# Kernel tuning notes

Hardware: AMD Instinct MI355X
Metric: run time of the kernel (lower is better)

Reference implementation:

```python
import jax, jax.numpy as jnp
import numpy as np

N, M = 50000, 12
ORIG, NBR_F, AF = 92, 41, 64
B, NA = 500, 100
NCONV = 3
BN_EPS = 1e-5


def _batchnorm(x, g, b):
    # training-mode batchnorm over axis 0 (biased variance, like torch)
    mu = jnp.mean(x, axis=0)
    var = jnp.mean((x - mu) ** 2, axis=0)
    return (x - mu) * jax.lax.rsqrt(var + BN_EPS) * g + b


def _conv_layer(atom, nbr_fea, nbr_idx, W, bW, g1, b1, g2, b2):
    n, m = nbr_idx.shape
    atom_nbr = atom[nbr_idx]                                   # [N,M,AF] gather
    center = jnp.broadcast_to(atom[:, None, :], (n, m, AF))
    total = jnp.concatenate([center, atom_nbr, nbr_fea], axis=2)  # [N,M,2AF+NBR_F]
    gated = jnp.einsum('nmf,of->nmo', total, W) + bW              # [N,M,2AF]
    gated = _batchnorm(gated.reshape(-1, 2 * AF), g1, b1).reshape(n, m, 2 * AF)
    filt, core = gated[..., :AF], gated[..., AF:]
    summed = jnp.sum(jax.nn.sigmoid(filt) * jax.nn.softplus(core), axis=1)  # [N,AF]
    summed = _batchnorm(summed, g2, b2)
    return jax.nn.softplus(atom + summed)


def setup_inputs() -> dict:
    key = jax.random.key(0)
    ks = jax.random.split(key, 12)
    inp = {
        'atom_fea': jax.random.normal(ks[0], (N, ORIG), jnp.float32),
        'nbr_fea': jax.random.normal(ks[1], (N, M, NBR_F), jnp.float32),
        'nbr_fea_idx': jax.random.randint(ks[2], (N, M), 0, N, jnp.int32),
        'crystal_atom_idx': jnp.arange(B * NA, dtype=jnp.int32).reshape(B, NA),
        'mask': jnp.ones((ORIG,), jnp.float32),
        'emb_W': jax.random.normal(ks[3], (AF, ORIG), jnp.float32) * 0.05,
        'conv_W': jax.random.normal(ks[4], (NCONV, 2 * AF, 2 * AF + NBR_F), jnp.float32) * 0.05,
        'conv_b': jnp.zeros((NCONV, 2 * AF), jnp.float32),
        'bn1_g': jnp.ones((NCONV, 2 * AF), jnp.float32),
        'bn1_b': jnp.zeros((NCONV, 2 * AF), jnp.float32),
        'bn2_g': jnp.ones((NCONV, AF), jnp.float32),
        'bn2_b': jnp.zeros((NCONV, AF), jnp.float32),
        'fc1_W': jax.random.normal(ks[5], (AF, AF), jnp.float32) * 0.05,
        'fc1_b': jnp.zeros((AF,), jnp.float32),
        'fc2_W': jax.random.normal(ks[6], (AF, AF), jnp.float32) * 0.05,
        'fc2_b': jnp.zeros((AF,), jnp.float32),
        'out_W': jax.random.normal(ks[7], (1, AF), jnp.float32) * 0.05,
        'out_b': jnp.zeros((1,), jnp.float32),
    }
    return inp


def reference(atom_fea, nbr_fea, nbr_fea_idx, crystal_atom_idx, mask, emb_W,
              conv_W, conv_b, bn1_g, bn1_b, bn2_g, bn2_b,
              fc1_W, fc1_b, fc2_W, fc2_b, out_W, out_b):
    x = atom_fea * mask                      # learned input mask
    atom_mask_feature = x
    h = x @ emb_W.T                          # embedding, no bias -> [N,AF]
    for i in range(NCONV):
        h = _conv_layer(h, nbr_fea, nbr_fea_idx, conv_W[i], conv_b[i],
                        bn1_g[i], bn1_b[i], bn2_g[i], bn2_b[i])
    g = h[crystal_atom_idx]                  # [B,NA,AF]
    norm = jnp.sqrt(jnp.sum(g * g, axis=-1, keepdims=True))
    g = g / jnp.maximum(norm, 1e-12)         # F.normalize p=2
    pooled = jnp.mean(g, axis=1)             # [B,AF]
    z = jax.nn.softplus(pooled @ fc1_W.T + fc1_b)
    z = jax.nn.softplus(z @ fc2_W.T + fc2_b)
    props = z @ out_W.T + out_b              # [B,1]
    return props, atom_mask_feature
```

## Files before the change

kernel.cpp:

```cpp
#include <hip/hip_runtime.h>
#include <hip/hip_bf16.h>
#include <stdint.h>

#define NN      50000
#define MMN     12
#define NMROWS  600000
#define ORIGF   92
#define NBRF    41
#define AFD     64
#define GCH     128
#define KTOT    169
#define BBC     500
#define NAA     100
#define BN_EPS  1e-5f
#define GROWS   96

typedef unsigned short u16;
typedef __attribute__((ext_vector_type(8))) short bf16x8;
typedef __attribute__((ext_vector_type(4))) float f32x4;

__device__ __forceinline__ float b2f(u16 u) {
    union { uint32_t i; float f; } v; v.i = ((uint32_t)u) << 16; return v.f;
}
__device__ __forceinline__ float hi2f(uint32_t p) {
    union { uint32_t i; float f; } v; v.i = p & 0xffff0000u; return v.f;
}
__device__ __forceinline__ u16 f2b(float f) {
    __hip_bfloat16 h = __float2bfloat16(f);
    return *(u16*)&h;
}
__device__ __forceinline__ float sp_f(float x) {
    return fmaxf(x, 0.f) + __logf(1.f + __expf(-fabsf(x)));
}
__device__ __forceinline__ float sigm_f(float x) {
    return __builtin_amdgcn_rcpf(1.f + __expf(-x));
}

__global__ void k_mask(const float* __restrict__ atom, const float* __restrict__ mask,
                       float* __restrict__ dout) {
    int i = blockIdx.x * blockDim.x + threadIdx.x;
    int stride = gridDim.x * blockDim.x;
    for (; i < NN * ORIGF; i += stride) {
        int k = i % ORIGF;
        dout[BBC + i] = atom[i] * mask[k];
    }
}

__global__ __launch_bounds__(256, 2) void k_emb(const float* __restrict__ atom,
                                                const float* __restrict__ mask,
                                                const float* __restrict__ embW,
                                                u16* __restrict__ h) {
    __shared__ float xs[4 * 96];
    int lane = threadIdx.x & 63;
    int w = threadIdx.x >> 6;
    float wr[ORIGF];
#pragma unroll
    for (int k = 0; k < ORIGF; ++k) wr[k] = embW[lane * ORIGF + k];
    float m1 = mask[lane];
    float m2 = (lane < ORIGF - 64) ? mask[64 + lane] : 0.f;
    for (int base = blockIdx.x * 4; base < NN; base += gridDim.x * 4) {
        int n = base + w;
        xs[w * 96 + lane] = atom[(size_t)n * ORIGF + lane] * m1;
        if (lane < ORIGF - 64)
            xs[w * 96 + 64 + lane] = atom[(size_t)n * ORIGF + 64 + lane] * m2;
        __syncthreads();
        float acc = 0.f;
#pragma unroll
        for (int k4 = 0; k4 < ORIGF / 4; ++k4) {
            float4 f = *(const float4*)&xs[w * 96 + 4 * k4];
            acc += f.x * wr[4*k4] + f.y * wr[4*k4+1] + f.z * wr[4*k4+2] + f.w * wr[4*k4+3];
        }
        h[(size_t)n * AFD + lane] = f2b(acc);
        __syncthreads();
    }
}

__global__ __launch_bounds__(256, 2) void k_cn(const u16* __restrict__ h,
                                               const float* __restrict__ convW,
                                               uint32_t* __restrict__ C32) {
    __shared__ float xs[2 * AFD];
    int lane = threadIdx.x & 63;
    int w = threadIdx.x >> 6;
    int half = w & 1;
    int sub = w >> 1;
    int koff = half * AFD;
    float wa[AFD], wb[AFD];
#pragma unroll
    for (int k = 0; k < AFD; ++k) {
        wa[k] = convW[lane * KTOT + koff + k];
        wb[k] = convW[(lane + 64) * KTOT + koff + k];
    }
    for (int base = blockIdx.x * 2; base < NN; base += gridDim.x * 2) {
        int n = base + sub;
        if (half == 0) xs[sub * AFD + lane] = b2f(h[(size_t)n * AFD + lane]);
        __syncthreads();
        float aa = 0.f, ab = 0.f;
#pragma unroll
        for (int k4 = 0; k4 < AFD / 4; ++k4) {
            float4 f = *(const float4*)&xs[sub * AFD + 4 * k4];
            aa += f.x * wa[4*k4] + f.y * wa[4*k4+1] + f.z * wa[4*k4+2] + f.w * wa[4*k4+3];
            ab += f.x * wb[4*k4] + f.y * wb[4*k4+1] + f.z * wb[4*k4+2] + f.w * wb[4*k4+3];
        }
        C32[(size_t)n * 128 + half * 64 + lane] = (uint32_t)f2b(aa) | ((uint32_t)f2b(ab) << 16);
        __syncthreads();
    }
}

__device__ __forceinline__ void stage_nbrf(const float* nbrf, int r0, float* fs) {
    const float4* src = (const float4*)(nbrf + (size_t)r0 * NBRF);
    for (int t = threadIdx.x; t < (GROWS * NBRF) / 4; t += 256) {
        float4 f = src[t];
        float vals[4] = {f.x, f.y, f.z, f.w};
#pragma unroll
        for (int j = 0; j < 4; ++j) {
            int e = t * 4 + j;
            int row = e / NBRF;
            int k = e - row * NBRF;
            fs[row * 44 + k] = vals[j];
        }
    }
}

template<bool STORE>
__global__ __launch_bounds__(256, 4) void k_gs3(
    const uint32_t* __restrict__ C32, const float* __restrict__ nbrf,
    const int* __restrict__ nbridx, const float* __restrict__ convW,
    const float* __restrict__ convb, float* __restrict__ stats,
    uint32_t* __restrict__ gated32)
{
    __shared__ __align__(16) u16 As[GROWS * 72];
    __shared__ __align__(16) u16 Ws[GCH * 72];
    __shared__ int nidx[GROWS];
    const int tid = threadIdx.x;
    const int lane = tid & 63;
    const int w = tid >> 6;
    const int lr = lane & 15;
    const int lg = lane >> 4;
    const int r0 = blockIdx.x * GROWS;
    const int nbase = blockIdx.x * (GROWS / MMN);

    const float* src = nbrf + (size_t)r0 * NBRF;
    for (int e = tid; e < GROWS * NBRF; e += 256) {
        int row = e / NBRF, k = e - row * NBRF;
        As[row * 72 + k] = f2b(src[e]);
    }
    for (int e = tid; e < GROWS * 23; e += 256) {
        int row = e / 23, k = 41 + (e - row * 23);
        As[row * 72 + k] = (k == 41) ? (u16)0x3F80 : (u16)0;
    }
    for (int e = tid; e < GCH * NBRF; e += 256) {
        int ch = e / NBRF, k = e - ch * NBRF;
        Ws[ch * 72 + k] = f2b(convW[ch * KTOT + 128 + k]);
    }
    for (int e = tid; e < GCH * 23; e += 256) {
        int ch = e / 23, k = 41 + (e - ch * 23);
        Ws[ch * 72 + k] = (k == 41) ? f2b(convb[ch]) : (u16)0;
    }
    if (tid < GROWS) nidx[tid] = nbridx[r0 + tid];
    __syncthreads();

    const u16* wlo = &Ws[(w * 16 + lr) * 72 + 8 * lg];
    const u16* whi = &Ws[(64 + w * 16 + lr) * 72 + 8 * lg];
    bf16x8 bl0 = *(const bf16x8*)(wlo);
    bf16x8 bl1 = *(const bf16x8*)(wlo + 32);
    bf16x8 bh0 = *(const bf16x8*)(whi);
    bf16x8 bh1 = *(const bf16x8*)(whi + 32);

    f32x4 acc[6][2];
    const f32x4 z = {0.f, 0.f, 0.f, 0.f};
#pragma unroll
    for (int mt = 0; mt < 6; ++mt) {
        const u16* ap = &As[(mt * 16 + lr) * 72 + 8 * lg];
        bf16x8 a0 = *(const bf16x8*)(ap);
        bf16x8 a1 = *(const bf16x8*)(ap + 32);
        acc[mt][0] = __builtin_amdgcn_mfma_f32_16x16x32_bf16(a1, bl1,
                     __builtin_amdgcn_mfma_f32_16x16x32_bf16(a0, bl0, z, 0, 0, 0), 0, 0, 0);
        acc[mt][1] = __builtin_amdgcn_mfma_f32_16x16x32_bf16(a1, bh1,
                     __builtin_amdgcn_mfma_f32_16x16x32_bf16(a0, bh0, z, 0, 0, 0), 0, 0, 0);
    }

    const int word = w * 16 + lr;
    float slo = 0.f, qlo = 0.f, shi = 0.f, qhi = 0.f;
#pragma unroll
    for (int mt = 0; mt < 6; ++mt) {
        uint32_t p1[4], p2[4];
#pragma unroll
        for (int rg = 0; rg < 4; ++rg) {
            int row = mt * 16 + 4 * lg + rg;
            int n = nbase + row / MMN;
            int j = nidx[row];
            p1[rg] = C32[(size_t)n * 128 + word];
            p2[rg] = C32[(size_t)j * 128 + 64 + word];
        }
#pragma unroll
        for (int rg = 0; rg < 4; ++rg) {
            float glo = acc[mt][0][rg] + b2f((u16)p1[rg]) + b2f((u16)p2[rg]);
            float ghi = acc[mt][1][rg] + hi2f(p1[rg]) + hi2f(p2[rg]);
            if (STORE) {
                int row = mt * 16 + 4 * lg + rg;
                gated32[(size_t)(r0 + row) * 64 + word] =
                    (uint32_t)f2b(glo) | ((uint32_t)f2b(ghi) << 16);
            }
            slo += glo; qlo = fmaf(glo, glo, qlo);
            shi += ghi; qhi = fmaf(ghi, ghi, qhi);
        }
    }
    slo += __shfl_xor(slo, 16, 64); slo += __shfl_xor(slo, 32, 64);
    qlo += __shfl_xor(qlo, 16, 64); qlo += __shfl_xor(qlo, 32, 64);
    shi += __shfl_xor(shi, 16, 64); shi += __shfl_xor(shi, 32, 64);
    qhi += __shfl_xor(qhi, 16, 64); qhi += __shfl_xor(qhi, 32, 64);
    if (lane < 16) {
        atomicAdd(&stats[word], slo);
        atomicAdd(&stats[128 + word], qlo);
        atomicAdd(&stats[64 + word], shi);
        atomicAdd(&stats[128 + 64 + word], qhi);
    }
}

__global__ void k_fin(float* __restrict__ stats, const float* __restrict__ gg,
                      const float* __restrict__ bb, int nch, float invcnt,
                      int sumoff, int sqoff, int scoff, int shoff) {
    int c = threadIdx.x;
    if (c < nch) {
        float mean = stats[sumoff + c] * invcnt;
        float var  = fmaxf(stats[sqoff + c] * invcnt - mean * mean, 0.f);
        float sc   = gg[c] * rsqrtf(var + BN_EPS);
        stats[scoff + c] = sc;
        stats[shoff + c] = bb[c] - mean * sc;
    }
}

__global__ __launch_bounds__(256) void k_acts(
    const uint32_t* __restrict__ gated32, float* __restrict__ stats,
    u16* __restrict__ summed)
{
    __shared__ float red[4][64][2];
    int lane = threadIdx.x & 63;
    int w = threadIdx.x >> 6;
    float sa = stats[384 + lane],      ba = stats[512 + lane];
    float sb = stats[384 + 64 + lane], bb = stats[512 + 64 + lane];
    int wave = blockIdx.x * 4 + w, nw = gridDim.x * 4;
    float s2 = 0.f, q2 = 0.f;
    for (int n = wave; n < NN; n += nw) {
        const uint32_t* gr = gated32 + (size_t)n * MMN * 64;
        float s = 0.f;
#pragma unroll
        for (int m = 0; m < MMN; ++m) {
            uint32_t p = gr[m * 64 + lane];
            float f1 = b2f((u16)p) * sa + ba;
            float cc = hi2f(p) * sb + bb;
            s += sigm_f(f1) * sp_f(cc);
        }
        summed[(size_t)n * AFD + lane] = f2b(s);
        s2 += s; q2 += s * s;
    }
    red[w][lane][0] = s2; red[w][lane][1] = q2;
    __syncthreads();
    if (threadIdx.x < 64) {
        int c = threadIdx.x;
        float a = 0, b = 0;
#pragma unroll
        for (int ww = 0; ww < 4; ++ww) { a += red[ww][c][0]; b += red[ww][c][1]; }
        atomicAdd(&stats[256 + c], a);
        atomicAdd(&stats[320 + c], b);
    }
}

__device__ __forceinline__ void edge_dot(const float* fr, const float* wfa,
                                         const float* wfb, float& aa, float& ab) {
#pragma unroll
    for (int k4 = 0; k4 < 10; ++k4) {
        float4 f = *(const float4*)&fr[4 * k4];
        aa += f.x * wfa[4*k4] + f.y * wfa[4*k4+1] + f.z * wfa[4*k4+2] + f.w * wfa[4*k4+3];
        ab += f.x * wfb[4*k4] + f.y * wfb[4*k4+1] + f.z * wfb[4*k4+2] + f.w * wfb[4*k4+3];
    }
    aa += fr[40] * wfa[40];
    ab += fr[40] * wfb[40];
}

__global__ __launch_bounds__(256) void k_act(
    const uint32_t* __restrict__ C32, const float* __restrict__ nbrf,
    const int* __restrict__ nbridx, const float* __restrict__ convW,
    const float* __restrict__ convb, float* __restrict__ stats,
    u16* __restrict__ summed)
{
    __shared__ float fs[GROWS * 44];
    __shared__ float red[4][64][2];
    int lane = threadIdx.x & 63;
    int w = threadIdx.x >> 6;
    int r0 = blockIdx.x * GROWS;
    stage_nbrf(nbrf, r0, fs);
    float wfa[NBRF], wfb[NBRF];
#pragma unroll
    for (int k = 0; k < NBRF; ++k) {
        wfa[k] = convW[lane * KTOT + 128 + k];
        wfb[k] = convW[(lane + 64) * KTOT + 128 + k];
    }
    float biasa = convb[lane], biasb = convb[64 + lane];
    float sa = stats[384 + lane],      ba = stats[512 + lane];
    float sb = stats[384 + 64 + lane], bb = stats[512 + 64 + lane];
    __syncthreads();
    float s2 = 0.f, q2 = 0.f;
    float s = 0.f;
    float c1a = 0.f, c1b = 0.f;
    for (int rr = 0; rr < 24; ++rr) {
        int rl = w * 24 + rr;
        int r = r0 + rl;
        if ((rr % MMN) == 0) {
            int n = r / MMN;
            uint32_t p1 = C32[(size_t)n * 128 + lane];
            c1a = b2f((u16)p1); c1b = b2f((u16)(p1 >> 16));
            s = 0.f;
        }
        int j = nbridx[r];
        uint32_t p2 = C32[(size_t)j * 128 + 64 + lane];
        float aa = c1a + b2f((u16)p2) + biasa;
        float ab = c1b + b2f((u16)(p2 >> 16)) + biasb;
        edge_dot(&fs[rl * 44], wfa, wfb, aa, ab);
        float f1 = aa * sa + ba;
        float cc = ab * sb + bb;
        s += sigm_f(f1) * sp_f(cc);
        if ((rr % MMN) == MMN - 1) {
            int n = r / MMN;
            summed[(size_t)n * AFD + lane] = f2b(s);
            s2 += s; q2 += s * s;
        }
    }
    red[w][lane][0] = s2; red[w][lane][1] = q2;
    __syncthreads();
    if (threadIdx.x < 64) {
        int c = threadIdx.x;
        float a = 0, b = 0;
#pragma unroll
        for (int ww = 0; ww < 4; ++ww) { a += red[ww][c][0]; b += red[ww][c][1]; }
        atomicAdd(&stats[256 + c], a);
        atomicAdd(&stats[320 + c], b);
    }
}

__global__ void k_update(u16* __restrict__ h, const u16* __restrict__ summed,
                         const float* __restrict__ stats) {
    int i = blockIdx.x * blockDim.x + threadIdx.x;
    int st = gridDim.x * blockDim.x;
    int c = threadIdx.x & 63;
    float sc = stats[640 + c], shf = stats[704 + c];
    for (; i < NN * AFD; i += st) {
        float x = b2f(h[i]) + b2f(summed[i]) * sc + shf;
        h[i] = f2b(sp_f(x));
    }
}

__global__ __launch_bounds__(256) void k_pool(const u16* __restrict__ h,
                                              const int* __restrict__ cry,
                                              float* __restrict__ pooled) {
    __shared__ float red[4][64];
    int lane = threadIdx.x & 63, w = threadIdx.x >> 6;
    int b = blockIdx.x;
    float acc = 0.f;
    for (int a = w; a < NAA; a += 4) {
        int idx = cry[b * NAA + a];
        float v = b2f(h[(size_t)idx * AFD + lane]);
        float s2 = v * v;
#pragma unroll
        for (int o = 32; o > 0; o >>= 1) s2 += __shfl_xor(s2, o, 64);
        acc += v / fmaxf(sqrtf(s2), 1e-12f);
    }
    red[w][lane] = acc;
    __syncthreads();
    if (threadIdx.x < 64) {
        float s = red[0][threadIdx.x] + red[1][threadIdx.x] +
                  red[2][threadIdx.x] + red[3][threadIdx.x];
        pooled[b * AFD + threadIdx.x] = s * (1.f / NAA);
    }
}

__global__ __launch_bounds__(64) void k_head(const float* __restrict__ pooled,
    const float* __restrict__ fc1W, const float* __restrict__ fc1b,
    const float* __restrict__ fc2W, const float* __restrict__ fc2b,
    const float* __restrict__ outW, const float* __restrict__ outb,
    float* __restrict__ props) {
    __shared__ float W1[64 * 65], W2[64 * 65], zbuf[64], pbuf[64];
    int l = threadIdx.x;
    for (int e = l; e < 64 * 64; e += 64) {
        int o = e >> 6, k = e & 63;
        W1[o * 65 + k] = fc1W[e];
        W2[o * 65 + k] = fc2W[e];
    }
    int b = blockIdx.x;
    pbuf[l] = pooled[b * AFD + l];
    __syncthreads();
    float acc = fc1b[l];
#pragma unroll
    for (int k = 0; k < 64; ++k) acc += pbuf[k] * W1[l * 65 + k];
    zbuf[l] = sp_f(acc);
    __syncthreads();
    acc = fc2b[l];
#pragma unroll
    for (int k = 0; k < 64; ++k) acc += zbuf[k] * W2[l * 65 + k];
    float v = sp_f(acc) * outW[l];
#pragma unroll
    for (int o = 32; o > 0; o >>= 1) v += __shfl_xor(v, o, 64);
    if (l == 0) props[b] = v + outb[0];
}

extern "C" void kernel_launch(void* const* d_in, const int* in_sizes, int n_in,
                              void* d_out, int out_size, void* d_ws, size_t ws_size,
                              hipStream_t stream) {
    const float* atom  = (const float*)d_in[0];
    const float* nbrf  = (const float*)d_in[1];
    const int* nbridx  = (const int*)d_in[2];
    const int* cry     = (const int*)d_in[3];
    const float* mask  = (const float*)d_in[4];
    const float* embW  = (const float*)d_in[5];
    const float* convW = (const float*)d_in[6];
    const float* convb = (const float*)d_in[7];
    const float* bn1g  = (const float*)d_in[8];
    const float* bn1b  = (const float*)d_in[9];
    const float* bn2g  = (const float*)d_in[10];
    const float* bn2b  = (const float*)d_in[11];
    const float* fc1W  = (const float*)d_in[12];
    const float* fc1b  = (const float*)d_in[13];
    const float* fc2W  = (const float*)d_in[14];
    const float* fc2b  = (const float*)d_in[15];
    const float* outW  = (const float*)d_in[16];
    const float* outb  = (const float*)d_in[17];

    char* ws = (char*)d_ws;
    float* stats    = (float*)ws;
    float* pooled   = (float*)(ws + 4096);
    u16*   h        = (u16*)(ws + (1u << 20));
    u16*   summed   = (u16*)(ws + (8u << 20));
    uint32_t* C32   = (uint32_t*)(ws + (16u << 20));
    uint32_t* gated32 = (uint32_t*)(ws + (48u << 20));
    const bool bigws = ws_size >= (size_t)(48u << 20) + 153600000u;

    float* out_props = (float*)d_out;

    k_mask<<<2048, 256, 0, stream>>>(atom, mask, (float*)d_out);
    k_emb<<<512, 256, 0, stream>>>(atom, mask, embW, h);
    for (int i = 0; i < 3; ++i) {
        hipMemsetAsync(stats, 0, 384 * sizeof(float), stream);
        k_cn<<<1024, 256, 0, stream>>>(h, convW + (size_t)i * GCH * KTOT, C32);
        if (bigws)
            k_gs3<true><<<NMROWS / GROWS, 256, 0, stream>>>(C32, nbrf, nbridx,
                convW + (size_t)i * GCH * KTOT, convb + (size_t)i * GCH, stats, gated32);
        else
            k_gs3<false><<<NMROWS / GROWS, 256, 0, stream>>>(C32, nbrf, nbridx,
                convW + (size_t)i * GCH * KTOT, convb + (size_t)i * GCH, stats, gated32);
        k_fin<<<1, 128, 0, stream>>>(stats, bn1g + (size_t)i * GCH, bn1b + (size_t)i * GCH,
                                     128, 1.f / NMROWS, 0, 128, 384, 512);
        if (bigws)
            k_acts<<<256, 256, 0, stream>>>(gated32, stats, summed);
        else
            k_act<<<NMROWS / GROWS, 256, 0, stream>>>(C32, nbrf, nbridx,
                convW + (size_t)i * GCH * KTOT, convb + (size_t)i * GCH, stats, summed);
        k_fin<<<1, 128, 0, stream>>>(stats, bn2g + (size_t)i * AFD, bn2b + (size_t)i * AFD,
                                     64, 1.f / NN, 256, 320, 640, 704);
        k_update<<<1024, 256, 0, stream>>>(h, summed, stats);
    }
    k_pool<<<BBC, 256, 0, stream>>>(h, cry, pooled);
    k_head<<<BBC, 64, 0, stream>>>(pooled, fc1W, fc1b, fc2W, fc2b, outW, outb, out_props);
}
```

Before: 1.105 ms.

## Stage neighbor and center C rows in LDS with coalesced gathers in gated kernel

The gated-GEMM kernel now gathers the neighbor half of C32 as full coalesced 64-word rows per wave and the 8 center rows per block into padded LDS. The epilogue then reads these from shared memory instead of issuing scattered per-element global loads. Weights are loaded straight into registers rather than through an LDS tile, the A tile is shrunk to 56 columns with vectorized float4 staging, and the activation kernel grid is raised from 256 to 1024 blocks. This adds LDS use (about 36 KB per block), which may limit occupancy.

```diff
diff --git a/kernel.cpp b/kernel.cpp
--- a/kernel.cpp
+++ b/kernel.cpp
@@ -122,57 +122,107 @@
 }
 
 template<bool STORE>
-__global__ __launch_bounds__(256, 4) void k_gs3(
+__global__ __launch_bounds__(256, 4) void k_gs4(
     const uint32_t* __restrict__ C32, const float* __restrict__ nbrf,
     const int* __restrict__ nbridx, const float* __restrict__ convW,
     const float* __restrict__ convb, float* __restrict__ stats,
     uint32_t* __restrict__ gated32)
 {
-    __shared__ __align__(16) u16 As[GROWS * 72];
-    __shared__ __align__(16) u16 Ws[GCH * 72];
-    __shared__ int nidx[GROWS];
-    const int tid = threadIdx.x;
+    __shared__ __align__(16) u16 As[GROWS * 56];
+    __shared__ uint32_t C2s[GROWS * 65];
+    __shared__ uint32_t C1s[8 * 65];
+    const int tid  = threadIdx.x;
     const int lane = tid & 63;
-    const int w = tid >> 6;
-    const int lr = lane & 15;
-    const int lg = lane >> 4;
-    const int r0 = blockIdx.x * GROWS;
+    const int w    = tid >> 6;
+    const int lr   = lane & 15;
+    const int lg   = lane >> 4;
+    const int r0    = blockIdx.x * GROWS;
     const int nbase = blockIdx.x * (GROWS / MMN);
-
-    const float* src = nbrf + (size_t)r0 * NBRF;
-    for (int e = tid; e < GROWS * NBRF; e += 256) {
-        int row = e / NBRF, k = e - row * NBRF;
-        As[row * 72 + k] = f2b(src[e]);
-    }
-    for (int e = tid; e < GROWS * 23; e += 256) {
-        int row = e / 23, k = 41 + (e - row * 23);
-        As[row * 72 + k] = (k == 41) ? (u16)0x3F80 : (u16)0;
-    }
-    for (int e = tid; e < GCH * NBRF; e += 256) {
-        int ch = e / NBRF, k = e - ch * NBRF;
-        Ws[ch * 72 + k] = f2b(convW[ch * KTOT + 128 + k]);
-    }
-    for (int e = tid; e < GCH * 23; e += 256) {
-        int ch = e / 23, k = 41 + (e - ch * 23);
-        Ws[ch * 72 + k] = (k == 41) ? f2b(convb[ch]) : (u16)0;
-    }
-    if (tid < GROWS) nidx[tid] = nbridx[r0 + tid];
-    __syncthreads();
-
-    const u16* wlo = &Ws[(w * 16 + lr) * 72 + 8 * lg];
-    const u16* whi = &Ws[(64 + w * 16 + lr) * 72 + 8 * lg];
-    bf16x8 bl0 = *(const bf16x8*)(wlo);
-    bf16x8 bl1 = *(const bf16x8*)(wlo + 32);
-    bf16x8 bh0 = *(const bf16x8*)(whi);
-    bf16x8 bh1 = *(const bf16x8*)(whi + 32);
+    const int rowb  = w * 24;
+
+    uint32_t c2v[12];
+#pragma unroll
+    for (int rr = 0; rr < 12; ++rr) {
+        int j = nbridx[r0 + rowb + rr];
+        c2v[rr] = C32[(size_t)j * 128 + 64 + lane];
+    }
+    uint32_t c1v[2];
+#pragma unroll
+    for (int q = 0; q < 2; ++q) {
+        int e = tid + q * 256;
+        c1v[q] = C32[(size_t)(nbase + (e >> 6)) * 128 + (e & 63)];
+    }
+    const float4* src4 = (const float4*)(nbrf + (size_t)r0 * NBRF);
+#pragma unroll
+    for (int it = 0; it < 4; ++it) {
+        int t = tid + it * 256;
+        if (it < 3 || t < 984) {
+            float4 f = src4[t];
+            float vals[4] = {f.x, f.y, f.z, f.w};
+#pragma unroll
+            for (int jj = 0; jj < 4; ++jj) {
+                int e = t * 4 + jj;
+                int row = e / NBRF;
+                int k = e - row * NBRF;
+                As[row * 56 + k] = f2b(vals[jj]);
+            }
+        }
+    }
+#pragma unroll
+    for (int rr = 0; rr < 12; ++rr) C2s[(rowb + rr) * 65 + lane] = c2v[rr];
+#pragma unroll
+    for (int rr = 0; rr < 12; ++rr) {
+        int j = nbridx[r0 + rowb + 12 + rr];
+        c2v[rr] = C32[(size_t)j * 128 + 64 + lane];
+    }
+#pragma unroll
+    for (int q = 0; q < 2; ++q) {
+        int e = tid + q * 256;
+        C1s[(e >> 6) * 65 + (e & 63)] = c1v[q];
+    }
+#pragma unroll
+    for (int it = 0; it < 6; ++it) {
+        int e = tid + it * 256;
+        if (it < 5 || e < 1440) {
+            int row = e / 15;
+            int k = 41 + (e - row * 15);
+            As[row * 56 + k] = (k == 41) ? (u16)0x3F80 : (u16)0;
+        }
+    }
+    const int chlo = w * 16 + lr;
+    const int chhi = chlo + 64;
+    const float* wlo = convW + (size_t)chlo * KTOT + 128;
+    const float* whi = convW + (size_t)chhi * KTOT + 128;
+    bf16x8 bl0, bh0;
+    bf16x8 bl1 = {0,0,0,0,0,0,0,0}, bh1 = {0,0,0,0,0,0,0,0};
+#pragma unroll
+    for (int e = 0; e < 8; ++e) {
+        bl0[e] = (short)f2b(wlo[8 * lg + e]);
+        bh0[e] = (short)f2b(whi[8 * lg + e]);
+    }
+    if (lg == 0) {
+#pragma unroll
+        for (int e = 0; e < 8; ++e) {
+            bl1[e] = (short)f2b(wlo[32 + e]);
+            bh1[e] = (short)f2b(whi[32 + e]);
+        }
+    } else if (lg == 1) {
+        bl1[0] = (short)f2b(wlo[40]); bl1[1] = (short)f2b(convb[chlo]);
+        bh1[0] = (short)f2b(whi[40]); bh1[1] = (short)f2b(convb[chhi]);
+    }
+#pragma unroll
+    for (int rr = 0; rr < 12; ++rr) C2s[(rowb + 12 + rr) * 65 + lane] = c2v[rr];
+    __syncthreads();
 
     f32x4 acc[6][2];
     const f32x4 z = {0.f, 0.f, 0.f, 0.f};
+    const bf16x8 zb = {0,0,0,0,0,0,0,0};
 #pragma unroll
     for (int mt = 0; mt < 6; ++mt) {
-        const u16* ap = &As[(mt * 16 + lr) * 72 + 8 * lg];
-        bf16x8 a0 = *(const bf16x8*)(ap);
-        bf16x8 a1 = *(const bf16x8*)(ap + 32);
+        const u16* ap = &As[(mt * 16 + lr) * 56 + 8 * lg];
+        bf16x8 a0 = *(const bf16x8*)ap;
+        bf16x8 a1 = zb;
+        if (lg < 3) a1 = *(const bf16x8*)(ap + 32);
         acc[mt][0] = __builtin_amdgcn_mfma_f32_16x16x32_bf16(a1, bl1,
                      __builtin_amdgcn_mfma_f32_16x16x32_bf16(a0, bl0, z, 0, 0, 0), 0, 0, 0);
         acc[mt][1] = __builtin_amdgcn_mfma_f32_16x16x32_bf16(a1, bh1,
@@ -183,21 +233,14 @@
     float slo = 0.f, qlo = 0.f, shi = 0.f, qhi = 0.f;
 #pragma unroll
     for (int mt = 0; mt < 6; ++mt) {
-        uint32_t p1[4], p2[4];
 #pragma unroll
         for (int rg = 0; rg < 4; ++rg) {
             int row = mt * 16 + 4 * lg + rg;
-            int n = nbase + row / MMN;
-            int j = nidx[row];
-            p1[rg] = C32[(size_t)n * 128 + word];
-            p2[rg] = C32[(size_t)j * 128 + 64 + word];
-        }
-#pragma unroll
-        for (int rg = 0; rg < 4; ++rg) {
-            float glo = acc[mt][0][rg] + b2f((u16)p1[rg]) + b2f((u16)p2[rg]);
-            float ghi = acc[mt][1][rg] + hi2f(p1[rg]) + hi2f(p2[rg]);
+            uint32_t p1 = C1s[(row / MMN) * 65 + word];
+            uint32_t p2 = C2s[row * 65 + word];
+            float glo = acc[mt][0][rg] + b2f((u16)p1) + b2f((u16)p2);
+            float ghi = acc[mt][1][rg] + hi2f(p1) + hi2f(p2);
             if (STORE) {
-                int row = mt * 16 + 4 * lg + rg;
                 gated32[(size_t)(r0 + row) * 64 + word] =
                     (uint32_t)f2b(glo) | ((uint32_t)f2b(ghi) << 16);
             }
@@ -442,15 +485,15 @@
         hipMemsetAsync(stats, 0, 384 * sizeof(float), stream);
         k_cn<<<1024, 256, 0, stream>>>(h, convW + (size_t)i * GCH * KTOT, C32);
         if (bigws)
-            k_gs3<true><<<NMROWS / GROWS, 256, 0, stream>>>(C32, nbrf, nbridx,
+            k_gs4<true><<<NMROWS / GROWS, 256, 0, stream>>>(C32, nbrf, nbridx,
                 convW + (size_t)i * GCH * KTOT, convb + (size_t)i * GCH, stats, gated32);
         else
-            k_gs3<false><<<NMROWS / GROWS, 256, 0, stream>>>(C32, nbrf, nbridx,
+            k_gs4<false><<<NMROWS / GROWS, 256, 0, stream>>>(C32, nbrf, nbridx,
                 convW + (size_t)i * GCH * KTOT, convb + (size_t)i * GCH, stats, gated32);
         k_fin<<<1, 128, 0, stream>>>(stats, bn1g + (size_t)i * GCH, bn1b + (size_t)i * GCH,
                                      128, 1.f / NMROWS, 0, 128, 384, 512);
         if (bigws)
-            k_acts<<<256, 256, 0, stream>>>(gated32, stats, summed);
+            k_acts<<<1024, 256, 0, stream>>>(gated32, stats, summed);
         else
             k_act<<<NMROWS / GROWS, 256, 0, stream>>>(C32, nbrf, nbridx,
                 convW + (size_t)i * GCH * KTOT, convb + (size_t)i * GCH, stats, summed);
```

Result: faster. 1.040 ms (-5.9%).
